# Kernel optimization log

Hardware: AMD Instinct MI355X
Metric: run time of the kernel (lower is better)

The kernel has to match this reference:

```python
import jax, jax.numpy as jnp
import numpy as np

B, L, H, D = 2, 2048, 8, 64
LOCAL_WINDOW = 32   # init arg
STRIDE = 64         # init arg


def _sparse_mask(L_Q, L_K, dtype):
    # Self-attention branch (L_Q == L_K): union of a local band of half-width
    # local_window//2 and strided diagonals at offsets that are multiples of (stride+1).
    i = jnp.arange(L_Q)[:, None]
    j = jnp.arange(L_K)[None, :]
    d = jnp.abs(i - j)
    band = d <= (LOCAL_WINDOW // 2)
    strided = (d % (STRIDE + 1)) == 0
    return (band | strided).astype(dtype)


def setup_inputs() -> dict:
    key = jax.random.key(0)
    kx, kq, kk, kv = jax.random.split(key, 4)
    x = jax.random.normal(kx, (B, L, H, D), jnp.float32)
    queries = jax.random.normal(kq, (B, L, H, D), jnp.float32)
    keys = jax.random.normal(kk, (B, L, H, D), jnp.float32)
    values = jax.random.normal(kv, (B, L, H, D), jnp.float32)
    # TriangularCausalMask: True on strictly upper triangle -> masked with -inf
    causal = jnp.triu(jnp.ones((L, L), dtype=bool), k=1)
    attn_mask = jnp.broadcast_to(causal[None, None], (B, 1, L, L))
    return {"x": x, "queries": queries, "keys": keys, "values": values,
            "attn_mask": attn_mask}


def reference(x, queries, keys, values, attn_mask):
    Bq, L_Q, Hh, Dh = queries.shape
    L_K = keys.shape[1]
    scale = 1.0 / np.sqrt(Dh)  # self.scale is None
    # [B,H,L_Q,L_K]
    scores = jnp.einsum('blhe,bshe->bhls', queries, keys)
    sparse = _sparse_mask(L_Q, L_K, scores.dtype)  # [L_Q, L_K]
    # NOTE: torch code ZEROES (not -inf) the non-sparse entries, then applies
    # the causal mask with -inf, then softmaxes scale*scores. Faithful here.
    scores = scores * sparse
    scores = jnp.where(attn_mask, -jnp.inf, scores)
    A = jax.nn.softmax(scale * scores, axis=-1)  # dropout = identity (eval)
    V = jnp.einsum('bhls,bshd->blhd', A, values)
    return V
```

## Files before the change

### kernel.cpp

```cpp
#include <hip/hip_runtime.h>

#define Bc 2
#define Lc 2048
#define Hc 8
#define Dc 64
#define TL 16
#define NT (Lc / TL)
#define RHD (Hc * Dc)
#define SP1 65
#define SCALE 0.125f

__global__ __launch_bounds__(256)
void dozer_chunk_sum(const float* __restrict__ V, float* __restrict__ partials) {
    const int bh = blockIdx.x;
    const int t  = blockIdx.y;
    const int b  = bh >> 3;
    const int h  = bh & 7;
    const int g  = threadIdx.x >> 6;
    const int d  = threadIdx.x & 63;
    const float* Vbh = V + (size_t)b * Lc * RHD + h * Dc;
    const int l0 = t * TL;
    float s = 0.f;
    for (int r = g; r < TL; r += 4)
        s += Vbh[(size_t)(l0 + r) * RHD + d];
    __shared__ float red[4][64];
    red[g][d] = s;
    __syncthreads();
    if (g == 0)
        partials[((size_t)bh * NT + t) * 64 + d] =
            red[0][d] + red[1][d] + red[2][d] + red[3][d];
}

__global__ __launch_bounds__(256)
void dozer_main(const float* __restrict__ Q, const float* __restrict__ K,
                const float* __restrict__ V, const float* __restrict__ partials,
                float* __restrict__ out) {
    const int bh   = blockIdx.x;
    const int t    = blockIdx.y;
    const int b    = bh >> 3;
    const int h    = bh & 7;
    const int tid  = threadIdx.x;
    const int wave = tid >> 6;
    const int lane = tid & 63;
    const int l0   = t * TL;

    const float* Qbh = Q + (size_t)b * Lc * RHD + h * Dc;
    const float* Kbh = K + (size_t)b * Lc * RHD + h * Dc;
    const float* Vbh = V + (size_t)b * Lc * RHD + h * Dc;

    __shared__ float Ptile[TL][64];
    __shared__ float red[4][64];

    float base = 0.f;
    if (partials) {
        const float* pb = partials + (size_t)bh * NT * 64;
        for (int c = wave; c < t; c += 4)
            base += pb[(size_t)c * 64 + lane];
    } else {
        for (int s = wave; s < l0; s += 4)
            base += Vbh[(size_t)s * RHD + lane];
    }
    red[wave][lane] = base;
    __syncthreads();
    if (wave == 0) {
        float s = red[0][lane] + red[1][lane] + red[2][lane] + red[3][lane];
        for (int r = 0; r < TL; ++r) {
            s += Vbh[(size_t)(l0 + r) * RHD + lane];
            Ptile[r][lane] = s;
        }
    }
    __syncthreads();

    const int p  = lane >> 4;
    const int dd = lane & 15;

    for (int rr = 0; rr < 4; ++rr) {
        const int r = wave * 4 + rr;
        const int l = l0 + r;
        const int nband = (l + 1 < 17) ? (l + 1) : 17;
        const int nstr  = l / SP1;
        const int npos  = nband + nstr;

        const float4 q4 = *(const float4*)&Qbh[(size_t)l * RHD + dd * 4];
        float4 acc = make_float4(0.f, 0.f, 0.f, 0.f);
        float  den = 0.f;

        #pragma unroll 2
        for (int i0 = 0; i0 < npos; i0 += 4) {
            const int pi = i0 + p;
            const bool ok = (pi < npos);
            int j;
            if (pi < nband) j = l - pi;
            else            j = l - SP1 * (pi - nband + 1);
            float dot = 0.f;
            float4 v4 = make_float4(0.f, 0.f, 0.f, 0.f);
            if (ok) {
                const float4 k4 = *(const float4*)&Kbh[(size_t)j * RHD + dd * 4];
                v4 = *(const float4*)&Vbh[(size_t)j * RHD + dd * 4];
                dot = q4.x * k4.x + q4.y * k4.y + q4.z * k4.z + q4.w * k4.w;
            }
            dot += __shfl_xor(dot, 1, 64);
            dot += __shfl_xor(dot, 2, 64);
            dot += __shfl_xor(dot, 4, 64);
            dot += __shfl_xor(dot, 8, 64);
            const float w = __expf(SCALE * dot) - 1.f;
            if (ok) {
                acc.x += w * v4.x; acc.y += w * v4.y;
                acc.z += w * v4.z; acc.w += w * v4.w;
                den += w;
            }
        }

        acc.x += __shfl_xor(acc.x, 16, 64); acc.x += __shfl_xor(acc.x, 32, 64);
        acc.y += __shfl_xor(acc.y, 16, 64); acc.y += __shfl_xor(acc.y, 32, 64);
        acc.z += __shfl_xor(acc.z, 16, 64); acc.z += __shfl_xor(acc.z, 32, 64);
        acc.w += __shfl_xor(acc.w, 16, 64); acc.w += __shfl_xor(acc.w, 32, 64);
        den   += __shfl_xor(den, 16, 64);   den   += __shfl_xor(den, 32, 64);

        const float inv = 1.f / ((float)(l + 1) + den);
        if (p == 0) {
            const float4 P4 = *(const float4*)&Ptile[r][dd * 4];
            float4 o;
            o.x = (P4.x + acc.x) * inv;
            o.y = (P4.y + acc.y) * inv;
            o.z = (P4.z + acc.z) * inv;
            o.w = (P4.w + acc.w) * inv;
            *(float4*)&out[((size_t)(b * Lc + l) * Hc + h) * Dc + dd * 4] = o;
        }
    }
}

extern "C" void kernel_launch(void* const* d_in, const int* in_sizes, int n_in,
                              void* d_out, int out_size, void* d_ws, size_t ws_size,
                              hipStream_t stream) {
    const float* Q = (const float*)d_in[1];
    const float* K = (const float*)d_in[2];
    const float* V = (const float*)d_in[3];
    float* out = (float*)d_out;

    const size_t need = (size_t)Bc * Hc * NT * 64 * sizeof(float);
    float* partials = (ws_size >= need) ? (float*)d_ws : nullptr;

    dim3 grid(Bc * Hc, NT);
    if (partials)
        dozer_chunk_sum<<<grid, 256, 0, stream>>>(V, partials);
    dozer_main<<<grid, 256, 0, stream>>>(Q, K, V, partials, out);
}
```

Measured before the change: 127.0 us.

## Use DPP row reductions, fixed-trip sparse loops, and parallel prefix tile

Replaces the shuffle-based 16-lane dot reduction with DPP row operations and splits the variable-length sparse loop into a fixed 16-entry band loop and a fixed 32-slot strided loop with clamped indices and predicated weights. This removes per-iteration divergence and loop-bound computation. The per-tile prefix sum of V is now computed by all four waves in parallel rather than serially by one wave. The scale is folded into q once per row. The cost is extra redundant loads for masked slots, since the strided loop always issues 32 slots even when few are valid.

```diff
diff --git a/kernel.cpp b/kernel.cpp
--- a/kernel.cpp
+++ b/kernel.cpp
@@ -9,6 +9,19 @@
 #define RHD (Hc * Dc)
 #define SP1 65
 #define SCALE 0.125f
+
+template <int CTRL>
+__device__ __forceinline__ float dpp_add(float x) {
+    int p = __builtin_amdgcn_update_dpp(0, __float_as_int(x), CTRL, 0xF, 0xF, true);
+    return x + __int_as_float(p);
+}
+__device__ __forceinline__ float row16_sum(float x) {
+    x = dpp_add<0xB1>(x);
+    x = dpp_add<0x4E>(x);
+    x = dpp_add<0x141>(x);
+    x = dpp_add<0x140>(x);
+    return x;
+}
 
 __global__ __launch_bounds__(256)
 void dozer_chunk_sum(const float* __restrict__ V, float* __restrict__ partials) {
@@ -49,27 +62,38 @@
     const float* Vbh = V + (size_t)b * Lc * RHD + h * Dc;
 
     __shared__ float Ptile[TL][64];
-    __shared__ float red[4][64];
+    __shared__ float red[8][64];
 
-    float base = 0.f;
-    if (partials) {
-        const float* pb = partials + (size_t)bh * NT * 64;
-        for (int c = wave; c < t; c += 4)
-            base += pb[(size_t)c * 64 + lane];
-    } else {
-        for (int s = wave; s < l0; s += 4)
-            base += Vbh[(size_t)s * RHD + lane];
+    {
+        const int d = lane;
+        float pbase = 0.f;
+        if (partials) {
+            const float* pb = partials + (size_t)bh * NT * 64;
+            for (int c = wave; c < t; c += 4)
+                pbase += pb[(size_t)c * 64 + d];
+        } else {
+            for (int s = wave; s < l0; s += 4)
+                pbase += Vbh[(size_t)s * RHD + d];
+        }
+        const float* vr = Vbh + (size_t)(l0 + 4 * wave) * RHD + d;
+        const float x0 = vr[0];
+        const float x1 = vr[RHD];
+        const float x2 = vr[2 * RHD];
+        const float x3 = vr[3 * RHD];
+        const float s0 = x0, s1 = s0 + x1, s2 = s1 + x2, s3 = s2 + x3;
+        red[wave][d]     = pbase;
+        red[4 + wave][d] = s3;
+        __syncthreads();
+        float base = red[0][d] + red[1][d] + red[2][d] + red[3][d];
+        if (wave > 0) base += red[4][d];
+        if (wave > 1) base += red[5][d];
+        if (wave > 2) base += red[6][d];
+        Ptile[4 * wave + 0][d] = base + s0;
+        Ptile[4 * wave + 1][d] = base + s1;
+        Ptile[4 * wave + 2][d] = base + s2;
+        Ptile[4 * wave + 3][d] = base + s3;
+        __syncthreads();
     }
-    red[wave][lane] = base;
-    __syncthreads();
-    if (wave == 0) {
-        float s = red[0][lane] + red[1][lane] + red[2][lane] + red[3][lane];
-        for (int r = 0; r < TL; ++r) {
-            s += Vbh[(size_t)(l0 + r) * RHD + lane];
-            Ptile[r][lane] = s;
-        }
-    }
-    __syncthreads();
 
     const int p  = lane >> 4;
     const int dd = lane & 15;
@@ -77,38 +101,48 @@
     for (int rr = 0; rr < 4; ++rr) {
         const int r = wave * 4 + rr;
         const int l = l0 + r;
-        const int nband = (l + 1 < 17) ? (l + 1) : 17;
-        const int nstr  = l / SP1;
-        const int npos  = nband + nstr;
 
-        const float4 q4 = *(const float4*)&Qbh[(size_t)l * RHD + dd * 4];
+        float4 q4 = *(const float4*)&Qbh[(size_t)l * RHD + dd * 4];
+        q4.x *= SCALE; q4.y *= SCALE; q4.z *= SCALE; q4.w *= SCALE;
+
         float4 acc = make_float4(0.f, 0.f, 0.f, 0.f);
         float  den = 0.f;
 
-        #pragma unroll 2
-        for (int i0 = 0; i0 < npos; i0 += 4) {
-            const int pi = i0 + p;
-            const bool ok = (pi < npos);
-            int j;
-            if (pi < nband) j = l - pi;
-            else            j = l - SP1 * (pi - nband + 1);
-            float dot = 0.f;
-            float4 v4 = make_float4(0.f, 0.f, 0.f, 0.f);
-            if (ok) {
-                const float4 k4 = *(const float4*)&Kbh[(size_t)j * RHD + dd * 4];
-                v4 = *(const float4*)&Vbh[(size_t)j * RHD + dd * 4];
-                dot = q4.x * k4.x + q4.y * k4.y + q4.z * k4.z + q4.w * k4.w;
-            }
-            dot += __shfl_xor(dot, 1, 64);
-            dot += __shfl_xor(dot, 2, 64);
-            dot += __shfl_xor(dot, 4, 64);
-            dot += __shfl_xor(dot, 8, 64);
-            const float w = __expf(SCALE * dot) - 1.f;
-            if (ok) {
-                acc.x += w * v4.x; acc.y += w * v4.y;
-                acc.z += w * v4.z; acc.w += w * v4.w;
-                den += w;
-            }
+        #pragma unroll
+        for (int it = 0; it < 4; ++it) {
+            const int pi = p + 4 * it;
+            const bool ok = (pi <= l);
+            int j = l - pi; if (j < 0) j = 0;
+            const float* Kr = Kbh + (size_t)j * RHD + dd * 4;
+            const float* Vr = Vbh + (size_t)j * RHD + dd * 4;
+            const float4 k4 = *(const float4*)Kr;
+            const float4 v4 = *(const float4*)Vr;
+            float dot = q4.x * k4.x + q4.y * k4.y + q4.z * k4.z + q4.w * k4.w;
+            dot = row16_sum(dot);
+            float w = __expf(dot) - 1.f;
+            w = ok ? w : 0.f;
+            acc.x += w * v4.x; acc.y += w * v4.y;
+            acc.z += w * v4.z; acc.w += w * v4.w;
+            den += w;
+        }
+
+        #pragma unroll 4
+        for (int it = 0; it < 8; ++it) {
+            const int f   = p + 4 * it;
+            int off = SP1 * f; if (off < 16) off = 16;
+            const bool ok = (off <= l);
+            int j = l - off; if (j < 0) j = 0;
+            const float* Kr = Kbh + (size_t)j * RHD + dd * 4;
+            const float* Vr = Vbh + (size_t)j * RHD + dd * 4;
+            const float4 k4 = *(const float4*)Kr;
+            const float4 v4 = *(const float4*)Vr;
+            float dot = q4.x * k4.x + q4.y * k4.y + q4.z * k4.z + q4.w * k4.w;
+            dot = row16_sum(dot);
+            float w = __expf(dot) - 1.f;
+            w = ok ? w : 0.f;
+            acc.x += w * v4.x; acc.y += w * v4.y;
+            acc.z += w * v4.z; acc.w += w * v4.w;
+            den += w;
         }
 
         acc.x += __shfl_xor(acc.x, 16, 64); acc.x += __shfl_xor(acc.x, 32, 64);
```

Measured after the change: 130.2 us. +2.5%, slower.
